# Kernel tuning notes

Hardware: AMD Instinct MI355X
Metric: run time of the kernel (lower is better)

Reference implementation:

```python
import jax, jax.numpy as jnp
import numpy as np

NUM_CLASSES = 19
EPS = 1e-8  # torch cosine_similarity eps


def setup_inputs() -> dict:
    key = jax.random.key(0)
    k1, k2 = jax.random.split(key)
    inputs = jax.random.normal(k1, (8, 256, 128, 128), dtype=jnp.float32)  # (B, D, H, W)
    targets = jax.random.randint(k2, (8, 128, 128), 0, NUM_CLASSES)        # (B, H, W)
    return {"inputs": inputs, "targets": targets}


def reference(inputs, targets):
    B, D, H, W = inputs.shape
    C = NUM_CLASSES
    # (N, D) pixel embeddings and (N,) labels
    feats = jnp.transpose(inputs, (0, 2, 3, 1)).reshape(-1, D)
    labels = targets.reshape(-1)

    # per-class centroids: sum of embeddings / max(count, 1)  (matches sum_pixel = max(mask.sum(), 1))
    counts = jax.ops.segment_sum(jnp.ones(labels.shape, jnp.float32), labels, num_segments=C)  # (C,)
    sums = jax.ops.segment_sum(feats, labels, num_segments=C)                                   # (C, D)
    centers = sums / jnp.maximum(counts, 1.0)[:, None]
    present = counts > 0  # classes absent from the batch are skipped in both loss terms

    # ---- sim_loss: sum over present classes of mean_{pixels of class i} (1 - cos(center_i, feat)) ----
    cen_px = centers[labels]                                   # (N, D)
    dot = jnp.sum(feats * cen_px, axis=1)
    n_f = jnp.sqrt(jnp.sum(feats * feats, axis=1))
    n_c = jnp.sqrt(jnp.sum(cen_px * cen_px, axis=1))
    cos_px = dot / jnp.maximum(n_f * n_c, EPS)
    per_class = jax.ops.segment_sum(1.0 - cos_px, labels, num_segments=C) / jnp.maximum(counts, 1.0)
    sim_loss = jnp.sum(jnp.where(present, per_class, 0.0))

    # ---- diff_loss: for each present i, mean_j over all C classes of
    #      (1 - cos(center_j, center_i)) if j == i else relu(cos(center_j, center_i)) ----
    n_cen = jnp.sqrt(jnp.sum(centers * centers, axis=1))       # (C,)
    S = (centers @ centers.T) / jnp.maximum(n_cen[:, None] * n_cen[None, :], EPS)  # (C, C)
    eye = jnp.eye(C, dtype=bool)
    per_pair = jnp.where(eye, 1.0 - S, jnp.maximum(S, 0.0))    # row i = losses vs class i
    per_i = jnp.mean(per_pair, axis=1)                          # mean reduction over C rows
    diff_loss = jnp.sum(jnp.where(present, per_i, 0.0))

    return jnp.reshape(diff_loss + sim_loss, (1,))  # torch returns a shape-(1,) tensor
```

## Files before the change

### kernel.cpp

```cpp
#include <hip/hip_runtime.h>
#include <math.h>

#define D_DIM 256
#define HW 16384
#define C 19
#define N_PX 131072
#define EPS 1e-8f

#define S_SUM 1048576.0f
#define IS_SUM (1.0f/1048576.0f)

#define OFF_SUMS_I   0
#define OFF_CNT_I    4864
#define OFF_DIFF_F   4883
#define OFF_NCEN_F   4884
#define OFF_ICNT_F   4903
#define OFF_CEN_F    4928
#define OFF_WSUM_F   9792
#define WS_ZERO      4883

__global__ void k0_zero(int* __restrict__ ws) {
    int i = blockIdx.x * blockDim.x + threadIdx.x;
    if (i < WS_ZERO) ws[i] = 0;
}

__global__ __launch_bounds__(256) void k1_sums(const float* __restrict__ in,
                                               const int* __restrict__ tgt,
                                               int* __restrict__ wsi) {
    __shared__ int s_sum[C * 33];
    __shared__ int s_cnt[C];
    const int tid = threadIdx.x;
    for (int i = tid; i < C * 33; i += 256) s_sum[i] = 0;
    if (tid < C) s_cnt[tid] = 0;
    __syncthreads();

    const int px0 = blockIdx.x << 9;
    const int b   = px0 >> 14;
    const int hw  = (px0 & (HW - 1)) + (tid << 1);
    const int d0  = blockIdx.y << 5;
    const int p   = px0 + (tid << 1);
    const int la = tgt[p], lb = tgt[p + 1];
    if (blockIdx.y == 0) {
        atomicAdd(&s_cnt[la], 1); atomicAdd(&s_cnt[lb], 1);
    }

    const float* base = in + (((size_t)(b * D_DIM + d0)) << 14) + hw;
    #pragma unroll
    for (int g = 0; g < 4; ++g) {
        float2 v[8];
        #pragma unroll
        for (int j = 0; j < 8; ++j)
            v[j] = *(const float2*)(base + ((size_t)(g * 8 + j) << 14));
        #pragma unroll
        for (int j = 0; j < 8; ++j) {
            const int dd = g * 8 + j;
            atomicAdd(&s_sum[la * 33 + dd], __float2int_rn(v[j].x * S_SUM));
            atomicAdd(&s_sum[lb * 33 + dd], __float2int_rn(v[j].y * S_SUM));
        }
    }
    __syncthreads();
    for (int i = tid; i < C * 32; i += 256) {
        int c = i >> 5, dd = i & 31;
        atomicAdd(&wsi[OFF_SUMS_I + c * D_DIM + d0 + dd], s_sum[c * 33 + dd]);
    }
    if (blockIdx.y == 0 && tid < C) atomicAdd(&wsi[OFF_CNT_I + tid], s_cnt[tid]);
}

__global__ __launch_bounds__(384) void k2_centers(int* __restrict__ wsi) {
    float* wsf = (float*)wsi;
    __shared__ float s_cen[C * 257];
    __shared__ float s_ncen[C];
    __shared__ float s_pair[C * C];
    __shared__ float s_red[C];
    const int tid = threadIdx.x;

    for (int i = tid; i < C * D_DIM; i += 384) {
        int c = i >> 8, d = i & 255;
        float cnt = (float)wsi[OFF_CNT_I + c];
        float cen = ((float)wsi[OFF_SUMS_I + i]) * IS_SUM / fmaxf(cnt, 1.f);
        wsf[OFF_CEN_F + i] = cen;
        s_cen[c * 257 + d] = cen;
    }
    __syncthreads();
    if (tid < C) {
        float nsq = 0.f;
        for (int d = 0; d < D_DIM; ++d) {
            float x = s_cen[tid * 257 + d];
            nsq += x * x;
        }
        float n = sqrtf(nsq);
        s_ncen[tid] = n;
        wsf[OFF_NCEN_F + tid] = n;
        float cnt = (float)wsi[OFF_CNT_I + tid];
        wsf[OFF_ICNT_F + tid] = 1.f / fmaxf(cnt, 1.f);
    }
    __syncthreads();
    if (tid < C * C) {
        int i = tid / C, j = tid % C;
        float dot = 0.f;
        for (int d = 0; d < D_DIM; ++d)
            dot += s_cen[i * 257 + d] * s_cen[j * 257 + d];
        float S = dot / fmaxf(s_ncen[i] * s_ncen[j], EPS);
        s_pair[tid] = (i == j) ? (1.f - S) : fmaxf(S, 0.f);
    }
    __syncthreads();
    if (tid < C) {
        float row = 0.f;
        for (int j = 0; j < C; ++j) row += s_pair[tid * C + j];
        s_red[tid] = (wsi[OFF_CNT_I + tid] > 0) ? (row / (float)C) : 0.f;
    }
    __syncthreads();
    if (tid == 0) {
        float diff = 0.f;
        for (int i = 0; i < C; ++i) diff += s_red[i];
        wsf[OFF_DIFF_F] = diff;
    }
}

__global__ __launch_bounds__(256) void k3_sim(const float* __restrict__ in,
                                              const int* __restrict__ tgt,
                                              int* __restrict__ wsi) {
    float* wsf = (float*)wsi;
    __shared__ float4 s_cen4[C * 65];
    __shared__ float s_ncen[C];
    __shared__ float s_icnt[C];
    const int tid = threadIdx.x;
    const float4* cen_g = (const float4*)(wsf + OFF_CEN_F);
    for (int i = tid; i < C * 64; i += 256) {
        int c = i >> 6, g = i & 63;
        s_cen4[c * 65 + g] = cen_g[c * 64 + g];
    }
    if (tid < C) {
        s_ncen[tid] = wsf[OFF_NCEN_F + tid];
        s_icnt[tid] = wsf[OFF_ICNT_F + tid];
    }
    __syncthreads();

    const int px0 = blockIdx.x << 9;
    const int b   = px0 >> 14;
    const int hw  = (px0 & (HW - 1)) + (tid << 1);
    const int p   = px0 + (tid << 1);
    const int la = tgt[p], lb = tgt[p + 1];
    const float4* ca = &s_cen4[la * 65];
    const float4* cb = &s_cen4[lb * 65];

    const float* base = in + (((size_t)(b * D_DIM)) << 14) + hw;
    float dta = 0.f, dtb = 0.f, nfa = 0.f, nfb = 0.f;
    #pragma unroll 4
    for (int g = 0; g < 32; ++g) {
        float2 v[8];
        #pragma unroll
        for (int j = 0; j < 8; ++j)
            v[j] = *(const float2*)(base + ((size_t)(g * 8 + j) << 14));
        float4 a0 = ca[g * 2], a1 = ca[g * 2 + 1];
        float4 b0 = cb[g * 2], b1 = cb[g * 2 + 1];
        dta += v[0].x * a0.x + v[1].x * a0.y + v[2].x * a0.z + v[3].x * a0.w
             + v[4].x * a1.x + v[5].x * a1.y + v[6].x * a1.z + v[7].x * a1.w;
        dtb += v[0].y * b0.x + v[1].y * b0.y + v[2].y * b0.z + v[3].y * b0.w
             + v[4].y * b1.x + v[5].y * b1.y + v[6].y * b1.z + v[7].y * b1.w;
        nfa += v[0].x * v[0].x + v[1].x * v[1].x + v[2].x * v[2].x + v[3].x * v[3].x
             + v[4].x * v[4].x + v[5].x * v[5].x + v[6].x * v[6].x + v[7].x * v[7].x;
        nfb += v[0].y * v[0].y + v[1].y * v[1].y + v[2].y * v[2].y + v[3].y * v[3].y
             + v[4].y * v[4].y + v[5].y * v[5].y + v[6].y * v[6].y + v[7].y * v[7].y;
    }

    const float cosa = dta / fmaxf(sqrtf(nfa) * s_ncen[la], EPS);
    const float cosb = dtb / fmaxf(sqrtf(nfb) * s_ncen[lb], EPS);
    float contrib = (1.f - cosa) * s_icnt[la] + (1.f - cosb) * s_icnt[lb];
    #pragma unroll
    for (int off = 32; off > 0; off >>= 1)
        contrib += __shfl_down(contrib, off, 64);
    if ((tid & 63) == 0)
        wsf[OFF_WSUM_F + blockIdx.x * 4 + (tid >> 6)] = contrib;
}

__global__ __launch_bounds__(256) void k4_final(const int* __restrict__ wsi,
                                                float* __restrict__ out) {
    const float* wsf = (const float*)wsi;
    __shared__ float s_w[4];
    float s = 0.f;
    for (int k = threadIdx.x; k < 1024; k += 256) s += wsf[OFF_WSUM_F + k];
    #pragma unroll
    for (int off = 32; off > 0; off >>= 1)
        s += __shfl_down(s, off, 64);
    if ((threadIdx.x & 63) == 0) s_w[threadIdx.x >> 6] = s;
    __syncthreads();
    if (threadIdx.x == 0)
        out[0] = s_w[0] + s_w[1] + s_w[2] + s_w[3] + wsf[OFF_DIFF_F];
}

extern "C" void kernel_launch(void* const* d_in, const int* in_sizes, int n_in,
                              void* d_out, int out_size, void* d_ws, size_t ws_size,
                              hipStream_t stream) {
    const float* in  = (const float*)d_in[0];
    const int*   tgt = (const int*)d_in[1];
    float* out = (float*)d_out;
    int*   wsi = (int*)d_ws;

    k0_zero<<<20, 256, 0, stream>>>(wsi);
    k1_sums<<<dim3(256, 8), 256, 0, stream>>>(in, tgt, wsi);
    k2_centers<<<1, 384, 0, stream>>>(wsi);
    k3_sim<<<256, 256, 0, stream>>>(in, tgt, wsi);
    k4_final<<<1, 256, 0, stream>>>(wsi, out);
}
```

Measured before the change: 233.6 us.

## Fold sim loss into single pass via per-class sums of normalized features

Rewrites the sim loss using linearity: the sum over pixels of cos(center, feat) equals the center dotted with the per-class sum of unit-normalized features, divided by the center norm. One pass over the input now accumulates both raw and normalized per-class sums in fixed-point shared-memory atomics, which removes the second full read of the input. The final kernel derives the sim and diff terms from those two small arrays. Each block reads its pixel tile twice (once for norms, once for scaled values), which will likely hit cache, and doubles the shared-memory atomic traffic. Fixed-point scaling at 2^24 adds some quantization and overflow risk.

```diff
diff --git a/kernel.cpp b/kernel.cpp
--- a/kernel.cpp
+++ b/kernel.cpp
@@ -7,186 +7,159 @@
 #define N_PX 131072
 #define EPS 1e-8f
 
-#define S_SUM 1048576.0f
-#define IS_SUM (1.0f/1048576.0f)
+#define S_SC  1048576.0f
+#define IS_S  (1.0f/1048576.0f)
+#define U_SC  16777216.0f
+#define IS_U  (1.0f/16777216.0f)
 
-#define OFF_SUMS_I   0
-#define OFF_CNT_I    4864
-#define OFF_DIFF_F   4883
-#define OFF_NCEN_F   4884
-#define OFF_ICNT_F   4903
-#define OFF_CEN_F    4928
-#define OFF_WSUM_F   9792
-#define WS_ZERO      4883
+#define OFF_S    0
+#define OFF_U    4864
+#define OFF_CNT  9728
+#define WS_ZERO  9747
 
 __global__ void k0_zero(int* __restrict__ ws) {
     int i = blockIdx.x * blockDim.x + threadIdx.x;
     if (i < WS_ZERO) ws[i] = 0;
 }
 
-__global__ __launch_bounds__(256) void k1_sums(const float* __restrict__ in,
+__global__ __launch_bounds__(256) void k1_pass(const float* __restrict__ in,
                                                const int* __restrict__ tgt,
                                                int* __restrict__ wsi) {
-    __shared__ int s_sum[C * 33];
+    __shared__ int sS[C * 257];
+    __shared__ int sU[C * 257];
     __shared__ int s_cnt[C];
+    __shared__ __align__(16) float s_nfp[128 * 4];
     const int tid = threadIdx.x;
-    for (int i = tid; i < C * 33; i += 256) s_sum[i] = 0;
+    const int q   = tid & 63;
+    const int dq  = tid >> 6;
+
+    for (int i = tid; i < C * 257; i += 256) { sS[i] = 0; sU[i] = 0; }
     if (tid < C) s_cnt[tid] = 0;
     __syncthreads();
 
-    const int px0 = blockIdx.x << 9;
+    const int px0 = blockIdx.x << 7;
     const int b   = px0 >> 14;
-    const int hw  = (px0 & (HW - 1)) + (tid << 1);
-    const int d0  = blockIdx.y << 5;
-    const int p   = px0 + (tid << 1);
+    const int hwq = (px0 & (HW - 1)) + (q << 1);
+    const int p   = px0 + (q << 1);
     const int la = tgt[p], lb = tgt[p + 1];
-    if (blockIdx.y == 0) {
-        atomicAdd(&s_cnt[la], 1); atomicAdd(&s_cnt[lb], 1);
-    }
+    if (dq == 0) { atomicAdd(&s_cnt[la], 1); atomicAdd(&s_cnt[lb], 1); }
 
-    const float* base = in + (((size_t)(b * D_DIM + d0)) << 14) + hw;
+    const float* base = in + (((size_t)(b * D_DIM + (dq << 6))) << 14) + hwq;
+
+    float nfa = 0.f, nfb = 0.f;
     #pragma unroll
-    for (int g = 0; g < 4; ++g) {
+    for (int g = 0; g < 8; ++g) {
         float2 v[8];
         #pragma unroll
         for (int j = 0; j < 8; ++j)
             v[j] = *(const float2*)(base + ((size_t)(g * 8 + j) << 14));
         #pragma unroll
         for (int j = 0; j < 8; ++j) {
-            const int dd = g * 8 + j;
-            atomicAdd(&s_sum[la * 33 + dd], __float2int_rn(v[j].x * S_SUM));
-            atomicAdd(&s_sum[lb * 33 + dd], __float2int_rn(v[j].y * S_SUM));
+            const int dd = (dq << 6) + g * 8 + j;
+            nfa += v[j].x * v[j].x; nfb += v[j].y * v[j].y;
+            atomicAdd(&sS[la * 257 + dd], __float2int_rn(v[j].x * S_SC));
+            atomicAdd(&sS[lb * 257 + dd], __float2int_rn(v[j].y * S_SC));
+        }
+    }
+    s_nfp[(q << 3) + dq]     = nfa;
+    s_nfp[(q << 3) + 4 + dq] = nfb;
+    __syncthreads();
+
+    const float4 na4 = *(const float4*)&s_nfp[q << 3];
+    const float4 nb4 = *(const float4*)&s_nfp[(q << 3) + 4];
+    const float nfs_a = na4.x + na4.y + na4.z + na4.w;
+    const float nfs_b = nb4.x + nb4.y + nb4.z + nb4.w;
+    const float sa = nfs_a > 0.f ? U_SC / sqrtf(nfs_a) : 0.f;
+    const float sb = nfs_b > 0.f ? U_SC / sqrtf(nfs_b) : 0.f;
+
+    #pragma unroll
+    for (int g = 0; g < 8; ++g) {
+        float2 v[8];
+        #pragma unroll
+        for (int j = 0; j < 8; ++j)
+            v[j] = *(const float2*)(base + ((size_t)(g * 8 + j) << 14));
+        #pragma unroll
+        for (int j = 0; j < 8; ++j) {
+            const int dd = (dq << 6) + g * 8 + j;
+            atomicAdd(&sU[la * 257 + dd], __float2int_rn(v[j].x * sa));
+            atomicAdd(&sU[lb * 257 + dd], __float2int_rn(v[j].y * sb));
         }
     }
     __syncthreads();
-    for (int i = tid; i < C * 32; i += 256) {
-        int c = i >> 5, dd = i & 31;
-        atomicAdd(&wsi[OFF_SUMS_I + c * D_DIM + d0 + dd], s_sum[c * 33 + dd]);
+
+    for (int i = tid; i < C * 256; i += 256) {
+        int c = i >> 8, d = i & 255;
+        atomicAdd(&wsi[OFF_S + i], sS[c * 257 + d]);
+        atomicAdd(&wsi[OFF_U + i], sU[c * 257 + d]);
     }
-    if (blockIdx.y == 0 && tid < C) atomicAdd(&wsi[OFF_CNT_I + tid], s_cnt[tid]);
+    if (tid < C) atomicAdd(&wsi[OFF_CNT + tid], s_cnt[tid]);
 }
 
-__global__ __launch_bounds__(384) void k2_centers(int* __restrict__ wsi) {
-    float* wsf = (float*)wsi;
-    __shared__ float s_cen[C * 257];
-    __shared__ float s_ncen[C];
+__global__ __launch_bounds__(512) void k2_final(const int* __restrict__ wsi,
+                                                float* __restrict__ out) {
+    __shared__ __align__(16) float s_cen[C * 260];
+    __shared__ __align__(16) float s_u[C * 260];
+    __shared__ float s_nc[C];
+    __shared__ float s_cntf[C];
     __shared__ float s_pair[C * C];
-    __shared__ float s_red[C];
+    __shared__ float s_sim[C];
     const int tid = threadIdx.x;
 
-    for (int i = tid; i < C * D_DIM; i += 384) {
+    if (tid < C) s_cntf[tid] = (float)wsi[OFF_CNT + tid];
+    __syncthreads();
+    for (int i = tid; i < C * 256; i += 512) {
         int c = i >> 8, d = i & 255;
-        float cnt = (float)wsi[OFF_CNT_I + c];
-        float cen = ((float)wsi[OFF_SUMS_I + i]) * IS_SUM / fmaxf(cnt, 1.f);
-        wsf[OFF_CEN_F + i] = cen;
-        s_cen[c * 257 + d] = cen;
+        float icnt = 1.f / fmaxf(s_cntf[c], 1.f);
+        s_cen[c * 260 + d] = (float)wsi[OFF_S + i] * IS_S * icnt;
+        s_u[c * 260 + d]   = (float)wsi[OFF_U + i] * IS_U;
     }
     __syncthreads();
     if (tid < C) {
         float nsq = 0.f;
         for (int d = 0; d < D_DIM; ++d) {
-            float x = s_cen[tid * 257 + d];
+            float x = s_cen[tid * 260 + d];
             nsq += x * x;
         }
-        float n = sqrtf(nsq);
-        s_ncen[tid] = n;
-        wsf[OFF_NCEN_F + tid] = n;
-        float cnt = (float)wsi[OFF_CNT_I + tid];
-        wsf[OFF_ICNT_F + tid] = 1.f / fmaxf(cnt, 1.f);
+        s_nc[tid] = sqrtf(nsq);
     }
     __syncthreads();
     if (tid < C * C) {
         int i = tid / C, j = tid % C;
+        const float4* ci = (const float4*)&s_cen[i * 260];
+        const float4* cj = (const float4*)&s_cen[j * 260];
         float dot = 0.f;
-        for (int d = 0; d < D_DIM; ++d)
-            dot += s_cen[i * 257 + d] * s_cen[j * 257 + d];
-        float S = dot / fmaxf(s_ncen[i] * s_ncen[j], EPS);
+        #pragma unroll 8
+        for (int k = 0; k < 64; ++k) {
+            float4 a = ci[k], bb = cj[k];
+            dot += a.x * bb.x + a.y * bb.y + a.z * bb.z + a.w * bb.w;
+        }
+        float S = dot / fmaxf(s_nc[i] * s_nc[j], EPS);
         s_pair[tid] = (i == j) ? (1.f - S) : fmaxf(S, 0.f);
+    } else if (tid >= 384 && tid < 384 + C) {
+        int i = tid - 384;
+        const float4* ci = (const float4*)&s_cen[i * 260];
+        const float4* ui = (const float4*)&s_u[i * 260];
+        float dot = 0.f;
+        #pragma unroll 8
+        for (int k = 0; k < 64; ++k) {
+            float4 a = ci[k], bb = ui[k];
+            dot += a.x * bb.x + a.y * bb.y + a.z * bb.z + a.w * bb.w;
+        }
+        s_sim[i] = (s_cntf[i] > 0.f)
+                 ? (1.f - dot / fmaxf(s_nc[i] * s_cntf[i], EPS)) : 0.f;
     }
     __syncthreads();
     if (tid < C) {
         float row = 0.f;
         for (int j = 0; j < C; ++j) row += s_pair[tid * C + j];
-        s_red[tid] = (wsi[OFF_CNT_I + tid] > 0) ? (row / (float)C) : 0.f;
+        s_pair[tid * C] = (s_cntf[tid] > 0.f) ? (row * (1.f / (float)C)) : 0.f;
     }
     __syncthreads();
     if (tid == 0) {
-        float diff = 0.f;
-        for (int i = 0; i < C; ++i) diff += s_red[i];
-        wsf[OFF_DIFF_F] = diff;
+        float tot = 0.f;
+        for (int i = 0; i < C; ++i) tot += s_pair[i * C] + s_sim[i];
+        out[0] = tot;
     }
-}
-
-__global__ __launch_bounds__(256) void k3_sim(const float* __restrict__ in,
-                                              const int* __restrict__ tgt,
-                                              int* __restrict__ wsi) {
-    float* wsf = (float*)wsi;
-    __shared__ float4 s_cen4[C * 65];
-    __shared__ float s_ncen[C];
-    __shared__ float s_icnt[C];
-    const int tid = threadIdx.x;
-    const float4* cen_g = (const float4*)(wsf + OFF_CEN_F);
-    for (int i = tid; i < C * 64; i += 256) {
-        int c = i >> 6, g = i & 63;
-        s_cen4[c * 65 + g] = cen_g[c * 64 + g];
-    }
-    if (tid < C) {
-        s_ncen[tid] = wsf[OFF_NCEN_F + tid];
-        s_icnt[tid] = wsf[OFF_ICNT_F + tid];
-    }
-    __syncthreads();
-
-    const int px0 = blockIdx.x << 9;
-    const int b   = px0 >> 14;
-    const int hw  = (px0 & (HW - 1)) + (tid << 1);
-    const int p   = px0 + (tid << 1);
-    const int la = tgt[p], lb = tgt[p + 1];
-    const float4* ca = &s_cen4[la * 65];
-    const float4* cb = &s_cen4[lb * 65];
-
-    const float* base = in + (((size_t)(b * D_DIM)) << 14) + hw;
-    float dta = 0.f, dtb = 0.f, nfa = 0.f, nfb = 0.f;
-    #pragma unroll 4
-    for (int g = 0; g < 32; ++g) {
-        float2 v[8];
-        #pragma unroll
-        for (int j = 0; j < 8; ++j)
-            v[j] = *(const float2*)(base + ((size_t)(g * 8 + j) << 14));
-        float4 a0 = ca[g * 2], a1 = ca[g * 2 + 1];
-        float4 b0 = cb[g * 2], b1 = cb[g * 2 + 1];
-        dta += v[0].x * a0.x + v[1].x * a0.y + v[2].x * a0.z + v[3].x * a0.w
-             + v[4].x * a1.x + v[5].x * a1.y + v[6].x * a1.z + v[7].x * a1.w;
-        dtb += v[0].y * b0.x + v[1].y * b0.y + v[2].y * b0.z + v[3].y * b0.w
-             + v[4].y * b1.x + v[5].y * b1.y + v[6].y * b1.z + v[7].y * b1.w;
-        nfa += v[0].x * v[0].x + v[1].x * v[1].x + v[2].x * v[2].x + v[3].x * v[3].x
-             + v[4].x * v[4].x + v[5].x * v[5].x + v[6].x * v[6].x + v[7].x * v[7].x;
-        nfb += v[0].y * v[0].y + v[1].y * v[1].y + v[2].y * v[2].y + v[3].y * v[3].y
-             + v[4].y * v[4].y + v[5].y * v[5].y + v[6].y * v[6].y + v[7].y * v[7].y;
-    }
-
-    const float cosa = dta / fmaxf(sqrtf(nfa) * s_ncen[la], EPS);
-    const float cosb = dtb / fmaxf(sqrtf(nfb) * s_ncen[lb], EPS);
-    float contrib = (1.f - cosa) * s_icnt[la] + (1.f - cosb) * s_icnt[lb];
-    #pragma unroll
-    for (int off = 32; off > 0; off >>= 1)
-        contrib += __shfl_down(contrib, off, 64);
-    if ((tid & 63) == 0)
-        wsf[OFF_WSUM_F + blockIdx.x * 4 + (tid >> 6)] = contrib;
-}
-
-__global__ __launch_bounds__(256) void k4_final(const int* __restrict__ wsi,
-                                                float* __restrict__ out) {
-    const float* wsf = (const float*)wsi;
-    __shared__ float s_w[4];
-    float s = 0.f;
-    for (int k = threadIdx.x; k < 1024; k += 256) s += wsf[OFF_WSUM_F + k];
-    #pragma unroll
-    for (int off = 32; off > 0; off >>= 1)
-        s += __shfl_down(s, off, 64);
-    if ((threadIdx.x & 63) == 0) s_w[threadIdx.x >> 6] = s;
-    __syncthreads();
-    if (threadIdx.x == 0)
-        out[0] = s_w[0] + s_w[1] + s_w[2] + s_w[3] + wsf[OFF_DIFF_F];
 }
 
 extern "C" void kernel_launch(void* const* d_in, const int* in_sizes, int n_in,
@@ -197,9 +170,7 @@
     float* out = (float*)d_out;
     int*   wsi = (int*)d_ws;
 
-    k0_zero<<<20, 256, 0, stream>>>(wsi);
-    k1_sums<<<dim3(256, 8), 256, 0, stream>>>(in, tgt, wsi);
-    k2_centers<<<1, 384, 0, stream>>>(wsi);
-    k3_sim<<<256, 256, 0, stream>>>(in, tgt, wsi);
-    k4_final<<<1, 256, 0, stream>>>(wsi, out);
+    k0_zero<<<39, 256, 0, stream>>>(wsi);
+    k1_pass<<<1024, 256, 0, stream>>>(in, tgt, wsi);
+    k2_final<<<1, 512, 0, stream>>>(wsi, out);
 }
```

Result: slower. 242.0 us (+3.6%).
